# Kernel tuning notes

Hardware: AMD Instinct MI355X
Metric: run time of the kernel (lower is better)

## Reference

```python
import jax, jax.numpy as jnp
import numpy as np
from jax import lax
from jax.scipy.special import logsumexp

B, T, L = 64, 256, 16          # batch, max words per sent, max chars per word
VC, DC, CH = 100, 50, 100      # char vocab, char emb dim, char cnn hidden
VW, DW = 50000, 300            # word vocab, word emb dim
VF, DF = 20, 20                # feature vocab, feature emb dim
H = 256                        # lstm hidden per direction (word_hidden_dim=512)
LAB = 50                       # label alphabet size
N = LAB + 2                    # +START, +STOP tags (NCRF++-style CRF)
START, STOP = N - 2, N - 1
IN = CH + DW + DF              # lstm input dim = 420


def setup_inputs():
    key = jax.random.key(0)
    k = jax.random.split(key, 16)
    p = 0.1
    # pack_padded_sequence requires lengths sorted descending; max length = T
    lens = jnp.sort(jax.random.randint(k[0], (B,), T // 2, T + 1))[::-1].at[0].set(T)
    mask = jnp.arange(T)[None, :] < lens[:, None]
    return dict(
        batch_word=jax.random.randint(k[1], (B, T), 0, VW),
        batch_features=jax.random.randint(k[2], (B, 1), 0, VF),
        batch_wordlen=lens,
        batch_char=jax.random.randint(k[3], (B * T, L), 0, VC),
        batch_charlen=jnp.full((B * T,), L, dtype=jnp.int32),
        batch_charrecover=jnp.arange(B * T),
        mask=mask,
        batch_label=jax.random.randint(k[4], (B, T), 0, LAB),
        char_emb=jax.random.normal(k[5], (VC, DC)) * p,
        conv_w=jax.random.normal(k[6], (CH, DC, 3)) * p,
        conv_b=jnp.zeros((CH,)),
        word_emb=jax.random.normal(k[7], (VW, DW)) * p,
        feat_emb=jax.random.normal(k[8], (VF, DF)) * p,
        w_ih_f=jax.random.normal(k[9], (4 * H, IN)) * p,
        w_hh_f=jax.random.normal(k[10], (4 * H, H)) * p,
        b_f=jnp.zeros((4 * H,)),
        w_ih_b=jax.random.normal(k[11], (4 * H, IN)) * p,
        w_hh_b=jax.random.normal(k[12], (4 * H, H)) * p,
        b_b=jnp.zeros((4 * H,)),
        proj_w=jax.random.normal(k[13], (N, 2 * H)) * p,
        proj_b=jnp.zeros((N,)),
        transitions=(jax.random.normal(k[14], (N, N)) * p)
            .at[:, START].set(-1e4).at[STOP, :].set(-1e4),
    )


def _lstm_dir(x_tb, m_tb, w_ih, w_hh, b, reverse):
    # x_tb: (T,B,IN), m_tb: (T,B,1) float; masked state update == packed-seq LSTM
    xs = jnp.einsum('tbi,gi->tbg', x_tb, w_ih) + b  # precomputed input proj
    def step(carry, inp):
        h, c = carry
        xt, mt = inp
        g = xt + h @ w_hh.T
        i, f, gg, o = jnp.split(g, 4, axis=-1)  # torch gate order i,f,g,o
        c_new = jax.nn.sigmoid(f) * c + jax.nn.sigmoid(i) * jnp.tanh(gg)
        h_new = jax.nn.sigmoid(o) * jnp.tanh(c_new)
        h = mt * h_new + (1 - mt) * h
        c = mt * c_new + (1 - mt) * c
        return (h, c), h
    init = (jnp.zeros((x_tb.shape[1], H), x_tb.dtype),
            jnp.zeros((x_tb.shape[1], H), x_tb.dtype))
    _, hs = lax.scan(step, init, (xs, m_tb), reverse=reverse)
    return hs  # (T,B,H)


def _emissions(batch_word, batch_features, batch_char, batch_charrecover, mask,
               char_emb, conv_w, conv_b, word_emb, feat_emb,
               w_ih_f, w_hh_f, b_f, w_ih_b, w_hh_b, b_b, proj_w, proj_b):
    maskf = mask.astype(jnp.float32)
    # char CNN (dropout = identity at eval time)
    ce = char_emb[batch_char].transpose(0, 2, 1)                     # (BT,DC,L)
    cc = lax.conv_general_dilated(ce, conv_w, (1,), [(1, 1)],
                                  dimension_numbers=('NCH', 'OIH', 'NCH'))
    cc = cc + conv_b[None, :, None]
    pooled = cc.max(axis=2)[batch_charrecover]                       # recover sort order
    char_feats = pooled.reshape(B, T, CH)
    feat_e = jnp.broadcast_to(feat_emb[batch_features], (B, T, DF))  # repeat_interleave
    x = jnp.concatenate([word_emb[batch_word], char_feats, feat_e], axis=2)
    x_tb, m_tb = x.transpose(1, 0, 2), maskf.T[:, :, None]
    hf = _lstm_dir(x_tb, m_tb, w_ih_f, w_hh_f, b_f, reverse=False)
    hb = _lstm_dir(x_tb, m_tb, w_ih_b, w_hh_b, b_b, reverse=True)
    # pad_packed zeroes padded outputs
    lstm_out = jnp.concatenate([hf, hb], axis=-1).transpose(1, 0, 2) * maskf[:, :, None]
    return lstm_out @ proj_w.T + proj_b                              # (B,T,N)


def _crf(feats, mask, batch_wordlen, batch_label, transitions):
    mb = mask.T[:, :, None]                                          # (T,B,1) bool
    s = feats[:, :, None, :] + transitions[None, None]               # (B,T,N,N): s[b,t,i,j]=feat[b,t,j]+T[i,j]
    st = jnp.moveaxis(s, 1, 0)                                       # (T,B,N,N)
    # ---- forward algorithm: log partition Z ----
    def fwd(a, inp):
        st_t, m = inp
        new = logsumexp(a[:, :, None] + st_t, axis=1)
        return jnp.where(m, new, a), None
    alpha, _ = lax.scan(fwd, st[0][:, START, :], (st[1:], mb[1:]))
    Z = logsumexp(alpha + transitions[:, STOP][None, :], axis=1)
    # ---- gold path score ----
    maskf = mask.astype(feats.dtype)
    emit = jnp.sum(jnp.take_along_axis(feats, batch_label[:, :, None], 2)[..., 0] * maskf, 1)
    tr = jnp.sum(transitions[batch_label[:, :-1], batch_label[:, 1:]] * maskf[:, 1:], 1)
    last_tag = jnp.take_along_axis(batch_label, (batch_wordlen - 1)[:, None], 1)[:, 0]
    gold = emit + tr + transitions[START, batch_label[:, 0]] + transitions[last_tag, STOP]
    loss = jnp.sum(Z - gold)
    # ---- viterbi decode ----
    def vstep(v, inp):
        st_t, m = inp
        cur = v[:, :, None] + st_t
        new, bp = cur.max(axis=1), cur.argmax(axis=1)
        v = jnp.where(m, new, v)
        bp = jnp.where(m, bp, jnp.arange(N)[None, :])  # identity bp on padding
        return v, bp
    v, bps = lax.scan(vstep, st[0][:, START, :], (st[1:], mb[1:]))
    term = v + transitions[:, STOP][None, :]
    best_last = jnp.argmax(term, axis=1)
    def back(tag, bp_t):
        prev = jnp.take_along_axis(bp_t, tag[:, None], 1)[:, 0]
        return prev, prev
    _, early = lax.scan(back, best_last, bps, reverse=True)          # tags for t=0..T-2
    path = jnp.concatenate([early, best_last[None]], 0).T            # (B,T)
    tag_seq = jnp.where(mask, path, 0)
    return loss, tag_seq


def reference(batch_word, batch_features, batch_wordlen, batch_char, batch_charlen,
              batch_charrecover, mask, batch_label,
              char_emb, conv_w, conv_b, word_emb, feat_emb,
              w_ih_f, w_hh_f, b_f, w_ih_b, w_hh_b, b_b, proj_w, proj_b, transitions):
    feats = _emissions(batch_word, batch_features, batch_char, batch_charrecover, mask,
                       char_emb, conv_w, conv_b, word_emb, feat_emb,
                       w_ih_f, w_hh_f, b_f, w_ih_b, w_hh_b, b_b, proj_w, proj_b)
    loss, tag_seq = _crf(feats, mask, batch_wordlen, batch_label, transitions)
    return loss, tag_seq
```

## Files before the change

### kernel.cpp

```cpp
#include <hip/hip_runtime.h>
#include <hip/hip_bf16.h>
#include <math.h>

#define BB 64
#define TT 256
#define LCH 16
#define DC 50
#define CHN 100
#define DW 300
#define DF 20
#define HID 256
#define G4 1024
#define INDIM 420
#define KPAD 448
#define NTAG 52
#define TSTART 50
#define TSTOP 51

static constexpr size_t OFF_POOL  = 0;
static constexpr size_t OFF_XH    = 6553600;
static constexpr size_t OFF_W16F  = 21233664;
static constexpr size_t OFF_W16B  = 22151168;
static constexpr size_t OFF_PW16  = 23068672;
static constexpr size_t OFF_HCAT  = 0;
static constexpr size_t OFF_XSF   = 34078720;
static constexpr size_t OFF_XSB   = 101187584;
static constexpr size_t OFF_FEATS = 168296448;
static constexpr size_t OFF_WPF   = 171704320;
static constexpr size_t OFF_WPB   = 172752896;
static constexpr size_t OFF_LOSSB = 173801472;
static constexpr size_t OFF_CTR   = 173801728;

typedef _Float16 v2h __attribute__((ext_vector_type(2)));
typedef _Float16 f16x8 __attribute__((ext_vector_type(8)));
typedef float f32x4 __attribute__((ext_vector_type(4)));
union UH2 { unsigned u; v2h h; };
__device__ __forceinline__ float fdot2u(unsigned a, unsigned b, float c) {
    UH2 x, y; x.u = a; y.u = b;
    return __builtin_amdgcn_fdot2(x.h, y.h, c, false);
}
__device__ __forceinline__ float dot8(uint4 w, uint4 h, float acc) {
    acc = fdot2u(w.x, h.x, acc);
    acc = fdot2u(w.y, h.y, acc);
    acc = fdot2u(w.z, h.z, acc);
    acc = fdot2u(w.w, h.w, acc);
    return acc;
}
#define KEEPU4(v) asm volatile("" : "+v"((v).x), "+v"((v).y), "+v"((v).z), "+v"((v).w))

__device__ __forceinline__ float sigm(float x) { return 1.0f / (1.0f + expf(-x)); }

#define CHARCNN_BLOCKS 2048
#define PREP_BLOCKS 5760

__device__ __forceinline__ void packh_one(const float* __restrict__ w,
                                          _Float16* __restrict__ wph, int e) {
    int r  = e & 7;
    int j  = (e >> 3) & 255;
    int k8 = (e >> 11) & 7;
    int g  = (e >> 14) & 3;
    int s  = (e >> 16) & 3;
    wph[e] = (_Float16)w[(g * 256 + j) * HID + (s * 64 + k8 * 8 + r)];
}
__device__ __forceinline__ void cvtw_one(const float* __restrict__ w,
                                         _Float16* __restrict__ wh, int e) {
    int row = e / KPAD, k = e % KPAD;
    wh[e] = (k < INDIM) ? (_Float16)w[row * INDIM + k] : (_Float16)0.f;
}

__global__ __launch_bounds__(256) void k_front(const int* __restrict__ bchar,
                                               const float* __restrict__ cemb,
                                               const float* __restrict__ cw,
                                               const float* __restrict__ cb,
                                               float* __restrict__ pooled,
                                               const float* __restrict__ whf,
                                               const float* __restrict__ whb,
                                               const float* __restrict__ wihf,
                                               const float* __restrict__ wihb,
                                               const float* __restrict__ pw,
                                               _Float16* __restrict__ wpf,
                                               _Float16* __restrict__ wpb,
                                               _Float16* __restrict__ wh16f,
                                               _Float16* __restrict__ wh16b,
                                               _Float16* __restrict__ pw16,
                                               unsigned* __restrict__ ctr) {
    __shared__ float cwsh[150][100];
    __shared__ float ET[2][DC][20];
    __shared__ int ids[2][LCH];
    int tid = threadIdx.x;
    if (blockIdx.x >= CHARCNN_BLOCKS) {
        int e = (blockIdx.x - CHARCNN_BLOCKS) * 256 + tid;
        if (e == 0) *ctr = 0u;
        if (e < 262144)                packh_one(whf, wpf, e);
        else if (e < 524288)           packh_one(whb, wpb, e - 262144);
        else if (e < 983040)           cvtw_one(wihf, wh16f, e - 524288);
        else if (e < 1441792)          cvtw_one(wihb, wh16b, e - 983040);
        else if (e < 1474560) {
            int p = e - 1441792;
            int row = p >> 9;
            pw16[p] = (row < NTAG) ? (_Float16)pw[p - (64 - NTAG) * 0 - (row - row) + (row * 512 + (p & 511)) - p + p] : (_Float16)0.f;
            pw16[p] = (row < NTAG) ? (_Float16)pw[row * 512 + (p & 511)] : (_Float16)0.f;
        }
        return;
    }
    int wbase = blockIdx.x * 8;
    for (int i = tid; i < 15000; i += 256) {
        int c = i / 150, row = i % 150;
        cwsh[row][c] = cw[i];
    }
    int half = tid >> 7, c = tid & 127;
    float bcv = (c < CHN) ? cb[c] : 0.f;
    for (int g = 0; g < 8; g += 2) {
        __syncthreads();
        if (tid < 32) ids[tid >> 4][tid & 15] = bchar[(wbase + g + (tid >> 4)) * LCH + (tid & 15)];
        __syncthreads();
        for (int s2 = tid; s2 < 2 * DC * 18; s2 += 256) {
            int w2 = s2 / 900, rem = s2 % 900;
            int d = rem / 18, l = rem % 18;
            float v = 0.f;
            if (l >= 1 && l <= 16) v = cemb[ids[w2][l - 1] * DC + d];
            ET[w2][d][l] = v;
        }
        __syncthreads();
        if (c < CHN) {
            float acc[16];
#pragma unroll
            for (int l = 0; l < 16; l++) acc[l] = 0.f;
            for (int d = 0; d < DC; d++) {
                float e[18];
                float4 t0 = *(const float4*)&ET[half][d][0];
                float4 t1 = *(const float4*)&ET[half][d][4];
                float4 t2 = *(const float4*)&ET[half][d][8];
                float4 t3 = *(const float4*)&ET[half][d][12];
                e[0]=t0.x; e[1]=t0.y; e[2]=t0.z; e[3]=t0.w;
                e[4]=t1.x; e[5]=t1.y; e[6]=t1.z; e[7]=t1.w;
                e[8]=t2.x; e[9]=t2.y; e[10]=t2.z; e[11]=t2.w;
                e[12]=t3.x; e[13]=t3.y; e[14]=t3.z; e[15]=t3.w;
                e[16]=ET[half][d][16]; e[17]=ET[half][d][17];
                float w0 = cwsh[d * 3 + 0][c];
                float w1 = cwsh[d * 3 + 1][c];
                float w2 = cwsh[d * 3 + 2][c];
#pragma unroll
                for (int l = 0; l < 16; l++)
                    acc[l] += w0 * e[l] + w1 * e[l + 1] + w2 * e[l + 2];
            }
            float m = acc[0];
#pragma unroll
            for (int l = 1; l < 16; l++) m = fmaxf(m, acc[l]);
            pooled[(wbase + g + half) * CHN + c] = m + bcv;
        }
    }
}

__global__ __launch_bounds__(256) void k_concat(const int* __restrict__ word,
                                                const int* __restrict__ featsidx,
                                                const int* __restrict__ recover,
                                                const float* __restrict__ wemb,
                                                const float* __restrict__ femb,
                                                const float* __restrict__ pooled,
                                                _Float16* __restrict__ xh) {
    int tid = threadIdx.x;
    for (int wi = 0; wi < 8; wi++) {
        int w = blockIdx.x * 8 + wi;
        int b = w >> 8;
        int wid = word[w];
        _Float16* xr = xh + (size_t)w * KPAD;
        for (int c = tid; c < DW; c += 256) xr[c] = (_Float16)wemb[(size_t)wid * DW + c];
        int rc = recover[w];
        if (tid < CHN) xr[DW + tid] = (_Float16)pooled[rc * CHN + tid];
        if (tid < DF)  xr[DW + CHN + tid] = (_Float16)femb[featsidx[b] * DF + tid];
        if (tid >= 100 && tid < 100 + (KPAD - INDIM)) xr[INDIM + (tid - 100)] = (_Float16)0.f;
    }
}

__global__ __launch_bounds__(256, 4) void k_gemm16b(const _Float16* __restrict__ A,
                                                    const _Float16* __restrict__ Bf,
                                                    const _Float16* __restrict__ Bb,
                                                    const float* __restrict__ biasf,
                                                    const float* __restrict__ biasb,
                                                    float* __restrict__ Cf,
                                                    float* __restrict__ Cb) {
    __shared__ __align__(16) _Float16 Asl[128 * 72];
    __shared__ __align__(16) _Float16 Bfl[64 * 72];
    __shared__ __align__(16) _Float16 Bbl[64 * 72];
    int tid = threadIdx.x;
    int wv = tid >> 6, l = tid & 63;
    int lm = l & 15, lk = l >> 4;
    int n0 = blockIdx.x * 64, m0 = blockIdx.y * 128;
    f32x4 z = {0.f, 0.f, 0.f, 0.f};
    f32x4 af0 = z, af1 = z, af2 = z, af3 = z;
    f32x4 ag0 = z, ag1 = z, ag2 = z, ag3 = z;
    f32x4 ab0 = z, ab1 = z, ab2 = z, ab3 = z;
    f32x4 ac0 = z, ac1 = z, ac2 = z, ac3 = z;
    for (int k0 = 0; k0 < KPAD; k0 += 64) {
        __syncthreads();
#pragma unroll
        for (int q = 0; q < 4; q++) {
            int ch = tid + q * 256;
            int r = ch >> 3, cc = ch & 7;
            ((uint4*)Asl)[r * 9 + cc] =
                *(const uint4*)&A[(size_t)(m0 + r) * KPAD + k0 + cc * 8];
        }
#pragma unroll
        for (int q = 0; q < 2; q++) {
            int ch = tid + q * 256;
            int r = ch >> 3, cc = ch & 7;
            ((uint4*)Bfl)[r * 9 + cc] =
                *(const uint4*)&Bf[(size_t)(n0 + r) * KPAD + k0 + cc * 8];
            ((uint4*)Bbl)[r * 9 + cc] =
                *(const uint4*)&Bb[(size_t)(n0 + r) * KPAD + k0 + cc * 8];
        }
        __syncthreads();
#pragma unroll
        for (int kstep = 0; kstep < 2; kstep++) {
            int kk = kstep * 4 + lk;
            f16x8 a0 = ((const f16x8*)Asl)[(wv * 32 + lm) * 9 + kk];
            f16x8 a1 = ((const f16x8*)Asl)[(wv * 32 + 16 + lm) * 9 + kk];
            f16x8 b0 = ((const f16x8*)Bfl)[(0 * 16 + lm) * 9 + kk];
            f16x8 b1 = ((const f16x8*)Bfl)[(1 * 16 + lm) * 9 + kk];
            f16x8 b2 = ((const f16x8*)Bfl)[(2 * 16 + lm) * 9 + kk];
            f16x8 b3 = ((const f16x8*)Bfl)[(3 * 16 + lm) * 9 + kk];
            f16x8 c0 = ((const f16x8*)Bbl)[(0 * 16 + lm) * 9 + kk];
            f16x8 c1 = ((const f16x8*)Bbl)[(1 * 16 + lm) * 9 + kk];
            f16x8 c2 = ((const f16x8*)Bbl)[(2 * 16 + lm) * 9 + kk];
            f16x8 c3 = ((const f16x8*)Bbl)[(3 * 16 + lm) * 9 + kk];
            af0 = __builtin_amdgcn_mfma_f32_16x16x32_f16(a0, b0, af0, 0, 0, 0);
            af1 = __builtin_amdgcn_mfma_f32_16x16x32_f16(a0, b1, af1, 0, 0, 0);
            af2 = __builtin_amdgcn_mfma_f32_16x16x32_f16(a0, b2, af2, 0, 0, 0);
            af3 = __builtin_amdgcn_mfma_f32_16x16x32_f16(a0, b3, af3, 0, 0, 0);
            ag0 = __builtin_amdgcn_mfma_f32_16x16x32_f16(a1, b0, ag0, 0, 0, 0);
            ag1 = __builtin_amdgcn_mfma_f32_16x16x32_f16(a1, b1, ag1, 0, 0, 0);
            ag2 = __builtin_amdgcn_mfma_f32_16x16x32_f16(a1, b2, ag2, 0, 0, 0);
            ag3 = __builtin_amdgcn_mfma_f32_16x16x32_f16(a1, b3, ag3, 0, 0, 0);
            ab0 = __builtin_amdgcn_mfma_f32_16x16x32_f16(a0, c0, ab0, 0, 0, 0);
            ab1 = __builtin_amdgcn_mfma_f32_16x16x32_f16(a0, c1, ab1, 0, 0, 0);
            ab2 = __builtin_amdgcn_mfma_f32_16x16x32_f16(a0, c2, ab2, 0, 0, 0);
            ab3 = __builtin_amdgcn_mfma_f32_16x16x32_f16(a0, c3, ab3, 0, 0, 0);
            ac0 = __builtin_amdgcn_mfma_f32_16x16x32_f16(a1, c0, ac0, 0, 0, 0);
            ac1 = __builtin_amdgcn_mfma_f32_16x16x32_f16(a1, c1, ac1, 0, 0, 0);
            ac2 = __builtin_amdgcn_mfma_f32_16x16x32_f16(a1, c2, ac2, 0, 0, 0);
            ac3 = __builtin_amdgcn_mfma_f32_16x16x32_f16(a1, c3, ac3, 0, 0, 0);
        }
    }
    f32x4 fa[2][4] = {{af0, af1, af2, af3}, {ag0, ag1, ag2, ag3}};
    f32x4 ba[2][4] = {{ab0, ab1, ab2, ab3}, {ac0, ac1, ac2, ac3}};
#pragma unroll
    for (int mi = 0; mi < 2; mi++) {
        int orow = m0 + wv * 32 + mi * 16 + lk * 4;
#pragma unroll
        for (int jn = 0; jn < 4; jn++) {
            int col = n0 + jn * 16 + lm;
            float bvf = biasf[col], bvb = biasb[col];
#pragma unroll
            for (int r = 0; r < 4; r++) {
                Cf[(size_t)(orow + r) * G4 + col] = fa[mi][jn][r] + bvf;
                Cb[(size_t)(orow + r) * G4 + col] = ba[mi][jn][r] + bvb;
            }
        }
    }
}

__global__ __launch_bounds__(1024, 4) void k_lstm(const float* __restrict__ xs_f,
                                               const float* __restrict__ xs_b,
                                               const _Float16* __restrict__ wh_f,
                                               const _Float16* __restrict__ wh_b,
                                               const int* __restrict__ wlen,
                                               _Float16* __restrict__ hcat) {
    int b = blockIdx.x & 63, d = blockIdx.x >> 6;
    const float* xs = d ? xs_b : xs_f;
    const uint4* wp4 = (const uint4*)(d ? wh_b : wh_f);
    int len = wlen[b];
    __shared__ uint4 olds4[8192];
    __shared__ _Float16 __align__(16) hh[256];
    __shared__ float part[4][4][256];
    int tid = threadIdx.x;
    int j = tid & 255, s = tid >> 8;
    const uint4* pi = wp4 + (size_t)((s * 4 + 0) * 8) * 256 + j;
    const uint4* pf = wp4 + (size_t)((s * 4 + 1) * 8) * 256 + j;
    uint4 wg[8];
    {
        const uint4* pg = wp4 + (size_t)((s * 4 + 2) * 8) * 256 + j;
        const uint4* po = wp4 + (size_t)((s * 4 + 3) * 8) * 256 + j;
#pragma unroll
        for (int k8 = 0; k8 < 8; k8++) {
            wg[k8] = pg[k8 * 256];
            olds4[k8 * 1024 + tid] = po[k8 * 256];
        }
    }
#pragma unroll
    for (int k8 = 0; k8 < 8; k8++) KEEPU4(wg[k8]);
    if (tid < 128) ((unsigned*)hh)[tid] = 0u;
    float c = 0.f;
    const uint4* hsh4 = (const uint4*)hh;
    __syncthreads();
    for (int ss = 0; ss < len; ++ss) {
        int t = d ? (len - 1 - ss) : ss;
        float xv0, xv1, xv2, xv3;
        if (tid < 256) {
            const float* xr = xs + (size_t)(b * TT + t) * G4;
            xv0 = xr[tid];
            xv1 = xr[256 + tid];
            xv2 = xr[512 + tid];
            xv3 = xr[768 + tid];
        }
        asm volatile("" : "+v"(pi), "+v"(pf));
        float a0 = 0.f, a1 = 0.f, a2 = 0.f, a3 = 0.f;
#pragma unroll
        for (int k8 = 0; k8 < 8; k8++) {
            uint4 h4 = hsh4[s * 8 + k8];
            uint4 wi = pi[k8 * 256];
            uint4 wf = pf[k8 * 256];
            uint4 wo = olds4[k8 * 1024 + tid];
            a0 = dot8(wi, h4, a0);
            a1 = dot8(wf, h4, a1);
            a2 = dot8(wg[k8], h4, a2);
            a3 = dot8(wo, h4, a3);
        }
        part[s][0][j] = a0;
        part[s][1][j] = a1;
        part[s][2][j] = a2;
        part[s][3][j] = a3;
        __syncthreads();
        if (tid < 256) {
            float s0 = part[0][0][tid] + part[1][0][tid] + part[2][0][tid] + part[3][0][tid] + xv0;
            float s1 = part[0][1][tid] + part[1][1][tid] + part[2][1][tid] + part[3][1][tid] + xv1;
            float s2 = part[0][2][tid] + part[1][2][tid] + part[2][2][tid] + part[3][2][tid] + xv2;
            float s3 = part[0][3][tid] + part[1][3][tid] + part[2][3][tid] + part[3][3][tid] + xv3;
            float ig = sigm(s0), fg = sigm(s1), zg = tanhf(s2), og = sigm(s3);
            c = fg * c + ig * zg;
            float h = og * tanhf(c);
            _Float16 h16 = (_Float16)h;
            hh[tid] = h16;
            hcat[(size_t)(b * TT + t) * 512 + d * 256 + tid] = h16;
        }
        __syncthreads();
    }
}

__global__ __launch_bounds__(256) void k_projm(const _Float16* __restrict__ A,
                                               const _Float16* __restrict__ Bw,
                                               const float* __restrict__ pb,
                                               float* __restrict__ feats) {
    __shared__ __align__(16) _Float16 Al[8 * 64 * 72];
    __shared__ __align__(16) _Float16 Bl[8 * 64 * 72];
    int tid = threadIdx.x;
    int wv = tid >> 6, l = tid & 63;
    int lm = l & 15, lk = l >> 4;
    int m0 = blockIdx.x * 64;
#pragma unroll
    for (int q = 0; q < 16; q++) {
        int ch = tid + q * 256;
        int r = ch >> 6;
        int rem = ch & 63;
        int cnk = rem >> 3, cc = rem & 7;
        ((uint4*)Al)[(cnk * 64 + r) * 9 + cc] =
            *(const uint4*)&A[(size_t)(m0 + r) * 512 + cnk * 64 + cc * 8];
        ((uint4*)Bl)[(cnk * 64 + r) * 9 + cc] =
            *(const uint4*)&Bw[(size_t)r * 512 + cnk * 64 + cc * 8];
    }
    __syncthreads();
    f32x4 z = {0.f, 0.f, 0.f, 0.f};
    f32x4 ac0 = z, ac1 = z, ac2 = z, ac3 = z;
#pragma unroll
    for (int cnk = 0; cnk < 8; cnk++) {
#pragma unroll
        for (int ks = 0; ks < 2; ks++) {
            int kk = ks * 4 + lk;
            f16x8 a  = ((const f16x8*)Al)[(cnk * 64 + wv * 16 + lm) * 9 + kk];
            f16x8 b0 = ((const f16x8*)Bl)[(cnk * 64 +  0 + lm) * 9 + kk];
            f16x8 b1 = ((const f16x8*)Bl)[(cnk * 64 + 16 + lm) * 9 + kk];
            f16x8 b2 = ((const f16x8*)Bl)[(cnk * 64 + 32 + lm) * 9 + kk];
            f16x8 b3 = ((const f16x8*)Bl)[(cnk * 64 + 48 + lm) * 9 + kk];
            ac0 = __builtin_amdgcn_mfma_f32_16x16x32_f16(a, b0, ac0, 0, 0, 0);
            ac1 = __builtin_amdgcn_mfma_f32_16x16x32_f16(a, b1, ac1, 0, 0, 0);
            ac2 = __builtin_amdgcn_mfma_f32_16x16x32_f16(a, b2, ac2, 0, 0, 0);
            ac3 = __builtin_amdgcn_mfma_f32_16x16x32_f16(a, b3, ac3, 0, 0, 0);
        }
    }
    f32x4 accs[4] = {ac0, ac1, ac2, ac3};
    int orow = m0 + wv * 16 + lk * 4;
#pragma unroll
    for (int jn = 0; jn < 4; jn++) {
        int col = jn * 16 + lm;
        if (col < NTAG) {
            float bv = pb[col];
#pragma unroll
            for (int r = 0; r < 4; r++)
                feats[(size_t)(orow + r) * NTAG + col] = accs[jn][r] + bv;
        }
    }
}

__global__ __launch_bounds__(64) void k_crf(const float* __restrict__ feats,
                                            const float* __restrict__ trans,
                                            const int* __restrict__ wlen,
                                            const int* __restrict__ blabel,
                                            float* __restrict__ lossb,
                                            float* __restrict__ outtags,
                                            unsigned* __restrict__ ctr,
                                            float* __restrict__ out) {
    __shared__ float Tm[NTAG * NTAG];
    __shared__ float st[NTAG];
    __shared__ unsigned char bp[TT - 1][NTAG];
    int bid = blockIdx.x;
    int b = bid & 63;
    bool vit = bid >= BB;
    int j = threadIdx.x;
    for (int s = j; s < NTAG * NTAG; s += 64) Tm[s] = trans[s];
    __builtin_amdgcn_wave_barrier();
    int len = wlen[b];
    const float* fb = feats + (size_t)b * TT * NTAG;
    if (j < NTAG) st[j] = fb[j] + Tm[TSTART * NTAG + j];
    __builtin_amdgcn_wave_barrier();
    if (!vit) {
        float frow = (j < NTAG && len > 1) ? fb[NTAG + j] : 0.f;
        for (int t = 1; t < len; t++) {
            float frow_nxt = (j < NTAG && t + 1 < len) ? fb[(size_t)(t + 1) * NTAG + j] : 0.f;
            float anew = 0.f;
            if (j < NTAG) {
                float ma = -1e30f, mb = -1e30f, mc = -1e30f, md = -1e30f;
                for (int i = 0; i < 13; i++) {
                    ma = fmaxf(ma, st[i]      + Tm[i * NTAG + j]);
                    mb = fmaxf(mb, st[i + 13] + Tm[(i + 13) * NTAG + j]);
                    mc = fmaxf(mc, st[i + 26] + Tm[(i + 26) * NTAG + j]);
                    md = fmaxf(md, st[i + 39] + Tm[(i + 39) * NTAG + j]);
                }
                float m1 = fmaxf(fmaxf(ma, mb), fmaxf(mc, md));
                float sa = 0.f, sb = 0.f, sc = 0.f, sd = 0.f;
                for (int i = 0; i < 13; i++) {
                    sa += expf(st[i]      + Tm[i * NTAG + j] - m1);
                    sb += expf(st[i + 13] + Tm[(i + 13) * NTAG + j] - m1);
                    sc += expf(st[i + 26] + Tm[(i + 26) * NTAG + j] - m1);
                    sd += expf(st[i + 39] + Tm[(i + 39) * NTAG + j] - m1);
                }
                anew = m1 + logf((sa + sb) + (sc + sd)) + frow;
            }
            __builtin_amdgcn_wave_barrier();
            if (j < NTAG) st[j] = anew;
            __builtin_amdgcn_wave_barrier();
            frow = frow_nxt;
        }
        float red = (j < NTAG) ? st[j] + Tm[j * NTAG + TSTOP] : -1e30f;
        float m1 = red;
#pragma unroll
        for (int m = 32; m; m >>= 1) m1 = fmaxf(m1, __shfl_xor(m1, m));
        float e = (j < NTAG) ? expf(red - m1) : 0.f;
        float ssum = e;
#pragma unroll
        for (int m = 32; m; m >>= 1) ssum += __shfl_xor(ssum, m);
        const int* lab = blabel + b * TT;
        float gpart = 0.f;
        for (int t = 1 + j; t < len; t += 64)
            gpart += Tm[lab[t - 1] * NTAG + lab[t]] + fb[(size_t)t * NTAG + lab[t]];
#pragma unroll
        for (int m = 32; m; m >>= 1) gpart += __shfl_xor(gpart, m);
        if (j == 0) {
            float Zg = m1 + logf(ssum);
            float goldv = Tm[TSTART * NTAG + lab[0]] + fb[lab[0]] + gpart
                        + Tm[lab[len - 1] * NTAG + TSTOP];
            lossb[b] = Zg - goldv;
            __threadfence();
            unsigned old = atomicAdd(ctr, 1u);
            if (old == BB - 1) {
                __threadfence();
                float stot = 0.f;
                for (int i = 0; i < BB; i++) stot += lossb[i];
                out[0] = stot;
            }
        }
    } else {
        float frow = (j < NTAG && len > 1) ? fb[NTAG + j] : 0.f;
        for (int t = 1; t < len; t++) {
            float frow_nxt = (j < NTAG && t + 1 < len) ? fb[(size_t)(t + 1) * NTAG + j] : 0.f;
            float vnew = 0.f;
            int arg = 0;
            if (j < NTAG) {
                float va = -1e30f, vb = -1e30f, vc = -1e30f, vd = -1e30f;
                int ia = 0, ib = 13, ic = 26, id2 = 39;
                for (int i = 0; i < 13; i++) {
                    float s0 = st[i]      + Tm[i * NTAG + j];        if (s0 > va) { va = s0; ia = i; }
                    float s1 = st[i + 13] + Tm[(i + 13) * NTAG + j]; if (s1 > vb) { vb = s1; ib = i + 13; }
                    float s2 = st[i + 26] + Tm[(i + 26) * NTAG + j]; if (s2 > vc) { vc = s2; ic = i + 26; }
                    float s3 = st[i + 39] + Tm[(i + 39) * NTAG + j]; if (s3 > vd) { vd = s3; id2 = i + 39; }
                }
                float vm = va; arg = ia;
                if (vb > vm) { vm = vb; arg = ib; }
                if (vc > vm) { vm = vc; arg = ic; }
                if (vd > vm) { vm = vd; arg = id2; }
                vnew = vm + frow;
            }
            __builtin_amdgcn_wave_barrier();
            if (j < NTAG) {
                st[j] = vnew;
                bp[t - 1][j] = (unsigned char)arg;
            }
            __builtin_amdgcn_wave_barrier();
            frow = frow_nxt;
        }
        if (j == 0) {
            int best = 0;
            float vm = st[0] + Tm[0 * NTAG + TSTOP];
            for (int i = 1; i < NTAG; i++) {
                float v = st[i] + Tm[i * NTAG + TSTOP];
                if (v > vm) { vm = v; best = i; }
            }
            float* ot = outtags + (size_t)b * TT;
            int tag = best;
            ot[len - 1] = (float)tag;
            for (int t = len - 2; t >= 0; t--) {
                tag = bp[t][tag];
                ot[t] = (float)tag;
            }
            for (int t = len; t < TT; t++) ot[t] = 0.f;
        }
    }
}

extern "C" void kernel_launch(void* const* d_in, const int* in_sizes, int n_in,
                              void* d_out, int out_size, void* d_ws, size_t ws_size,
                              hipStream_t stream) {
    const int* batch_word     = (const int*)d_in[0];
    const int* batch_features = (const int*)d_in[1];
    const int* batch_wordlen  = (const int*)d_in[2];
    const int* batch_char     = (const int*)d_in[3];
    const int* batch_recover  = (const int*)d_in[5];
    const int* batch_label    = (const int*)d_in[7];
    const float* char_emb = (const float*)d_in[8];
    const float* conv_w   = (const float*)d_in[9];
    const float* conv_b   = (const float*)d_in[10];
    const float* word_emb = (const float*)d_in[11];
    const float* feat_emb = (const float*)d_in[12];
    const float* w_ih_f   = (const float*)d_in[13];
    const float* w_hh_f   = (const float*)d_in[14];
    const float* b_f      = (const float*)d_in[15];
    const float* w_ih_b   = (const float*)d_in[16];
    const float* w_hh_b   = (const float*)d_in[17];
    const float* b_b      = (const float*)d_in[18];
    const float* proj_w   = (const float*)d_in[19];
    const float* proj_b   = (const float*)d_in[20];
    const float* trans    = (const float*)d_in[21];

    char* ws = (char*)d_ws;
    float* pooled   = (float*)(ws + OFF_POOL);
    _Float16* xh    = (_Float16*)(ws + OFF_XH);
    _Float16* wh16f = (_Float16*)(ws + OFF_W16F);
    _Float16* wh16b = (_Float16*)(ws + OFF_W16B);
    _Float16* pw16  = (_Float16*)(ws + OFF_PW16);
    _Float16* hcat  = (_Float16*)(ws + OFF_HCAT);
    float* xs_f   = (float*)(ws + OFF_XSF);
    float* xs_b   = (float*)(ws + OFF_XSB);
    float* feats  = (float*)(ws + OFF_FEATS);
    _Float16* wh_f = (_Float16*)(ws + OFF_WPF);
    _Float16* wh_b = (_Float16*)(ws + OFF_WPB);
    float* lossb  = (float*)(ws + OFF_LOSSB);
    unsigned* ctr = (unsigned*)(ws + OFF_CTR);

    k_front<<<CHARCNN_BLOCKS + PREP_BLOCKS, 256, 0, stream>>>(
        batch_char, char_emb, conv_w, conv_b, pooled,
        w_hh_f, w_hh_b, w_ih_f, w_ih_b, proj_w,
        wh_f, wh_b, wh16f, wh16b, pw16, ctr);
    k_concat<<<(BB * TT) / 8, 256, 0, stream>>>(batch_word, batch_features, batch_recover,
                                                word_emb, feat_emb, pooled, xh);
    k_gemm16b<<<dim3(G4 / 64, (BB * TT) / 128), 256, 0, stream>>>(xh, wh16f, wh16b,
                                                                  b_f, b_b, xs_f, xs_b);
    k_lstm<<<128, 1024, 0, stream>>>(xs_f, xs_b, wh_f, wh_b, batch_wordlen, hcat);
    k_projm<<<(BB * TT) / 64, 256, 0, stream>>>(hcat, pw16, proj_b, feats);
    k_crf<<<2 * BB, 64, 0, stream>>>(feats, trans, batch_wordlen, batch_label,
                                     lossb, (float*)d_out + 1, ctr, (float*)d_out);
}
```

Baseline: 1.499 ms.

## Prefetch GEMM tiles into registers, use fast exp/log in CRF, tidy char-CNN loads

The input-projection GEMM now issues its global loads for the next K-tile into registers before the barrier, then writes them to shared memory, so global latency can overlap other waves' work. The CRF forward recursion swaps expf/logf for the faster, lower-precision __expf/__logf intrinsics. The char-CNN embedding staging loop changes its index decomposition so consecutive threads read consecutive embedding dims, and a duplicated dead pw16 store is removed. Fast-math intrinsics may slightly change loss precision, and the register staging adds register pressure.

```diff
diff --git a/kernel.cpp b/kernel.cpp
--- a/kernel.cpp
+++ b/kernel.cpp
@@ -98,7 +98,6 @@
         else if (e < 1474560) {
             int p = e - 1441792;
             int row = p >> 9;
-            pw16[p] = (row < NTAG) ? (_Float16)pw[p - (64 - NTAG) * 0 - (row - row) + (row * 512 + (p & 511)) - p + p] : (_Float16)0.f;
             pw16[p] = (row < NTAG) ? (_Float16)pw[row * 512 + (p & 511)] : (_Float16)0.f;
         }
         return;
@@ -116,7 +115,7 @@
         __syncthreads();
         for (int s2 = tid; s2 < 2 * DC * 18; s2 += 256) {
             int w2 = s2 / 900, rem = s2 % 900;
-            int d = rem / 18, l = rem % 18;
+            int l = rem / DC, d = rem % DC;
             float v = 0.f;
             if (l >= 1 && l <= 16) v = cemb[ids[w2][l - 1] * DC + d];
             ET[w2][d][l] = v;
@@ -192,23 +191,30 @@
     f32x4 ag0 = z, ag1 = z, ag2 = z, ag3 = z;
     f32x4 ab0 = z, ab1 = z, ab2 = z, ab3 = z;
     f32x4 ac0 = z, ac1 = z, ac2 = z, ac3 = z;
+    int ra_[4], rca_[4];
+#pragma unroll
+    for (int q = 0; q < 4; q++) { int ch = tid + q * 256; ra_[q] = ch >> 3; rca_[q] = ch & 7; }
+    int rb_[2], rcb_[2];
+#pragma unroll
+    for (int q = 0; q < 2; q++) { int ch = tid + q * 256; rb_[q] = ch >> 3; rcb_[q] = ch & 7; }
     for (int k0 = 0; k0 < KPAD; k0 += 64) {
-        __syncthreads();
-#pragma unroll
-        for (int q = 0; q < 4; q++) {
-            int ch = tid + q * 256;
-            int r = ch >> 3, cc = ch & 7;
-            ((uint4*)Asl)[r * 9 + cc] =
-                *(const uint4*)&A[(size_t)(m0 + r) * KPAD + k0 + cc * 8];
-        }
+        uint4 va[4], vbf[2], vbb[2];
+#pragma unroll
+        for (int q = 0; q < 4; q++)
+            va[q] = *(const uint4*)&A[(size_t)(m0 + ra_[q]) * KPAD + k0 + rca_[q] * 8];
 #pragma unroll
         for (int q = 0; q < 2; q++) {
-            int ch = tid + q * 256;
-            int r = ch >> 3, cc = ch & 7;
-            ((uint4*)Bfl)[r * 9 + cc] =
-                *(const uint4*)&Bf[(size_t)(n0 + r) * KPAD + k0 + cc * 8];
-            ((uint4*)Bbl)[r * 9 + cc] =
-                *(const uint4*)&Bb[(size_t)(n0 + r) * KPAD + k0 + cc * 8];
+            vbf[q] = *(const uint4*)&Bf[(size_t)(n0 + rb_[q]) * KPAD + k0 + rcb_[q] * 8];
+            vbb[q] = *(const uint4*)&Bb[(size_t)(n0 + rb_[q]) * KPAD + k0 + rcb_[q] * 8];
+        }
+        __syncthreads();
+#pragma unroll
+        for (int q = 0; q < 4; q++)
+            ((uint4*)Asl)[ra_[q] * 9 + rca_[q]] = va[q];
+#pragma unroll
+        for (int q = 0; q < 2; q++) {
+            ((uint4*)Bfl)[rb_[q] * 9 + rcb_[q]] = vbf[q];
+            ((uint4*)Bbl)[rb_[q] * 9 + rcb_[q]] = vbb[q];
         }
         __syncthreads();
 #pragma unroll
@@ -428,12 +434,12 @@
                 float m1 = fmaxf(fmaxf(ma, mb), fmaxf(mc, md));
                 float sa = 0.f, sb = 0.f, sc = 0.f, sd = 0.f;
                 for (int i = 0; i < 13; i++) {
-                    sa += expf(st[i]      + Tm[i * NTAG + j] - m1);
-                    sb += expf(st[i + 13] + Tm[(i + 13) * NTAG + j] - m1);
-                    sc += expf(st[i + 26] + Tm[(i + 26) * NTAG + j] - m1);
-                    sd += expf(st[i + 39] + Tm[(i + 39) * NTAG + j] - m1);
+                    sa += __expf(st[i]      + Tm[i * NTAG + j] - m1);
+                    sb += __expf(st[i + 13] + Tm[(i + 13) * NTAG + j] - m1);
+                    sc += __expf(st[i + 26] + Tm[(i + 26) * NTAG + j] - m1);
+                    sd += __expf(st[i + 39] + Tm[(i + 39) * NTAG + j] - m1);
                 }
-                anew = m1 + logf((sa + sb) + (sc + sd)) + frow;
+                anew = m1 + __logf((sa + sb) + (sc + sd)) + frow;
             }
             __builtin_amdgcn_wave_barrier();
             if (j < NTAG) st[j] = anew;
@@ -444,7 +450,7 @@
         float m1 = red;
 #pragma unroll
         for (int m = 32; m; m >>= 1) m1 = fmaxf(m1, __shfl_xor(m1, m));
-        float e = (j < NTAG) ? expf(red - m1) : 0.f;
+        float e = (j < NTAG) ? __expf(red - m1) : 0.f;
         float ssum = e;
 #pragma unroll
         for (int m = 32; m; m >>= 1) ssum += __shfl_xor(ssum, m);
@@ -455,7 +461,7 @@
 #pragma unroll
         for (int m = 32; m; m >>= 1) gpart += __shfl_xor(gpart, m);
         if (j == 0) {
-            float Zg = m1 + logf(ssum);
+            float Zg = m1 + __logf(ssum);
             float goldv = Tm[TSTART * NTAG + lab[0]] + fb[lab[0]] + gpart
                         + Tm[lab[len - 1] * NTAG + TSTOP];
             lossb[b] = Zg - goldv;
```

New measurement: 1.364 ms. -9.0%, faster.
